# Performance work log

Measured on AMD Instinct MI355X. Metric: run time of the kernel, lower is better.

Reference implementation:

```python
import jax, jax.numpy as jnp
import numpy as np

B, T, E, H = 1024, 200, 128, 128
N_ITEMS, N_CATS = 100000, 1000
LN_EPS = 1e-5


def _prelu(x, a):
    return jnp.where(x >= 0, x, a * x)


def _layernorm(x, g, b):
    m = x.mean(-1, keepdims=True)
    v = ((x - m) ** 2).mean(-1, keepdims=True)
    return (x - m) / jnp.sqrt(v + LN_EPS) * g + b


def setup_inputs() -> dict:
    key = jax.random.key(0)
    it = iter(jax.random.split(key, 64))
    nx = lambda: next(it)
    def lin(out_d, in_d):
        s = 1.0 / np.sqrt(in_d)
        return jax.random.uniform(nx(), (out_d, in_d), jnp.float32, -s, s)
    inp = {}
    inp['behavior_ids'] = jax.random.randint(nx(), (B, T), 0, N_ITEMS)
    inp['candidate_id'] = jax.random.randint(nx(), (B,), 0, N_ITEMS)
    inp['candidate_cat'] = jax.random.randint(nx(), (B,), 0, N_CATS)
    inp['dense_features'] = jax.random.normal(nx(), (B, 5), jnp.float32)
    inp['item_emb'] = (jax.random.normal(nx(), (N_ITEMS, E), jnp.float32) * 0.01).at[0].set(0.0)
    inp['cat_emb'] = (jax.random.normal(nx(), (N_CATS, E // 2), jnp.float32) * 0.01).at[0].set(0.0)
    # nn.GRU params (gate order r,z,n)
    inp['gru_wih'] = lin(3 * H, E)
    inp['gru_whh'] = lin(3 * H, H)
    inp['gru_bih'] = jnp.zeros((3 * H,), jnp.float32)
    inp['gru_bhh'] = jnp.zeros((3 * H,), jnp.float32)
    # auxiliary_net: Linear(H,E) -> ReLU -> Linear(E,1)
    inp['aux_w1'] = lin(E, H); inp['aux_b1'] = jnp.zeros((E,), jnp.float32)
    inp['aux_w2'] = lin(1, E); inp['aux_b2'] = jnp.zeros((1,), jnp.float32)
    # attention_mlp: Linear(3H,64) -> PReLU -> Linear(64,1)
    inp['att_w1'] = lin(64, 3 * H); inp['att_b1'] = jnp.zeros((64,), jnp.float32)
    inp['att_a'] = jnp.array(0.25, jnp.float32)
    inp['att_w2'] = lin(1, 64); inp['att_b2'] = jnp.zeros((1,), jnp.float32)
    # AUGRU gates: Linear(2H, H) each
    inp['wz'] = lin(H, 2 * H); inp['bz'] = jnp.zeros((H,), jnp.float32)
    inp['wr'] = lin(H, 2 * H); inp['br'] = jnp.zeros((H,), jnp.float32)
    inp['wh'] = lin(H, 2 * H); inp['bh'] = jnp.zeros((H,), jnp.float32)
    # dense_proj Linear(5,32)
    inp['dp_w'] = lin(32, 5); inp['dp_b'] = jnp.zeros((32,), jnp.float32)
    # MLP: 352 -> 256 -> 128 -> 64, each Linear + LayerNorm + PReLU
    dims = [H + E + E // 2 + 32, 256, 128, 64]
    for i in range(3):
        inp[f'm_w{i+1}'] = lin(dims[i + 1], dims[i])
        inp[f'm_b{i+1}'] = jnp.zeros((dims[i + 1],), jnp.float32)
        inp[f'ln_g{i+1}'] = jnp.ones((dims[i + 1],), jnp.float32)
        inp[f'ln_b{i+1}'] = jnp.zeros((dims[i + 1],), jnp.float32)
        inp[f'pa{i+1}'] = jnp.array(0.25, jnp.float32)
    # 3 task heads Linear(64,1), stacked
    inp['heads_w'] = lin(3, 64); inp['heads_b'] = jnp.zeros((3,), jnp.float32)
    return inp


def _forward_core(behavior_ids, candidate_id, candidate_cat, dense_features,
                  item_emb, cat_emb, gru_wih, gru_whh, gru_bih, gru_bhh,
                  aux_w1, aux_b1, aux_w2, aux_b2,
                  att_w1, att_b1, att_a, att_w2, att_b2,
                  wz, bz, wr, br, wh, bh, dp_w, dp_b,
                  m_w1, m_b1, ln_g1, ln_b1, pa1,
                  m_w2, m_b2, ln_g2, ln_b2, pa2,
                  m_w3, m_b3, ln_g3, ln_b3, pa3,
                  heads_w, heads_b):
    beh = item_emb[behavior_ids]            # [B,T,E]
    cand = item_emb[candidate_id]           # [B,E]
    catv = cat_emb[candidate_cat]           # [B,E//2]
    Bsz = beh.shape[0]
    Hd = gru_whh.shape[1]
    h0 = jnp.zeros((Bsz, Hd), beh.dtype)
    # --- interest extractor GRU (cuDNN GRU math, gate order r,z,n) ---
    xp = jnp.einsum('bte,ge->btg', beh, gru_wih) + gru_bih  # [B,T,3H]
    def gru_step(h, x):
        hp = h @ gru_whh.T + gru_bhh
        xr, xz, xn = jnp.split(x, 3, -1)
        hr, hz, hn = jnp.split(hp, 3, -1)
        r = jax.nn.sigmoid(xr + hr)
        z = jax.nn.sigmoid(xz + hz)
        n = jnp.tanh(xn + r * hn)
        hnew = (1 - z) * n + z * h
        return hnew, hnew
    _, hs = jax.lax.scan(gru_step, h0, jnp.swapaxes(xp, 0, 1))
    hs = jnp.swapaxes(hs, 0, 1)             # [B,T,H]
    # --- auxiliary logits ---
    aux = jax.nn.relu(hs[:, :-1] @ aux_w1.T + aux_b1) @ aux_w2.T + aux_b2  # [B,T-1,1]
    # --- attention (embed_dim == hidden_size so cand_proj == candidate_emb) ---
    ce = cand[:, None, :]
    att_in = jnp.concatenate([hs, jnp.broadcast_to(ce, hs.shape), hs * ce], -1)  # [B,T,3H]
    scores = (_prelu(att_in @ att_w1.T + att_b1, att_a) @ att_w2.T + att_b2)[..., 0]
    att = jax.nn.softmax(scores, axis=-1)   # [B,T]
    # --- AUGRU: attention-modulated update gate ---
    def augru_step(h, xs):
        x, a = xs                           # x: [B,H], a: [B]
        comb = jnp.concatenate([x, h], -1)
        z = jax.nn.sigmoid(comb @ wz.T + bz)
        r = jax.nn.sigmoid(comb @ wr.T + br)
        comb_r = jnp.concatenate([x, r * h], -1)
        ht = jnp.tanh(comb_r @ wh.T + bh)
        zp = a[:, None] * z
        return (1 - zp) * h + zp * ht, None
    hT, _ = jax.lax.scan(augru_step, h0, (jnp.swapaxes(hs, 0, 1), att.T))
    # --- fusion MLP (dropout is identity in eval) ---
    dense_out = dense_features @ dp_w.T + dp_b
    x = jnp.concatenate([hT, cand, catv, dense_out], -1)  # [B,352]
    for (w, b, g, be, a) in ((m_w1, m_b1, ln_g1, ln_b1, pa1),
                             (m_w2, m_b2, ln_g2, ln_b2, pa2),
                             (m_w3, m_b3, ln_g3, ln_b3, pa3)):
        x = _prelu(_layernorm(x @ w.T + b, g, be), a)
    preds = jax.nn.sigmoid(x @ heads_w.T + heads_b)  # [B,3] == 3 heads of [B,1]
    return preds, aux


def reference(behavior_ids, candidate_id, candidate_cat, dense_features,
              item_emb, cat_emb, gru_wih, gru_whh, gru_bih, gru_bhh,
              aux_w1, aux_b1, aux_w2, aux_b2,
              att_w1, att_b1, att_a, att_w2, att_b2,
              wz, bz, wr, br, wh, bh, dp_w, dp_b,
              m_w1, m_b1, ln_g1, ln_b1, pa1,
              m_w2, m_b2, ln_g2, ln_b2, pa2,
              m_w3, m_b3, ln_g3, ln_b3, pa3,
              heads_w, heads_b):
    return _forward_core(behavior_ids, candidate_id, candidate_cat, dense_features,
                         item_emb, cat_emb, gru_wih, gru_whh, gru_bih, gru_bhh,
                         aux_w1, aux_b1, aux_w2, aux_b2,
                         att_w1, att_b1, att_a, att_w2, att_b2,
                         wz, bz, wr, br, wh, bh, dp_w, dp_b,
                         m_w1, m_b1, ln_g1, ln_b1, pa1,
                         m_w2, m_b2, ln_g2, ln_b2, pa2,
                         m_w3, m_b3, ln_g3, ln_b3, pa3,
                         heads_w, heads_b)
```

## Files before the change

### kernel.cpp

```cpp
#include <hip/hip_runtime.h>


typedef __bf16 bf16;
typedef float f32x4 __attribute__((ext_vector_type(4)));
typedef __bf16 bf16x8 __attribute__((ext_vector_type(8)));
typedef __bf16 bf16x4 __attribute__((ext_vector_type(4)));

#define MFMA16(a, b, c) __builtin_amdgcn_mfma_f32_16x16x32_bf16((a), (b), (c), 0, 0, 0)

#define BATCH 1024
#define SEQT 200
#define F32_ONE 0x3F800000u

__device__ __forceinline__ float sigm(float x) {
  return __builtin_amdgcn_rcpf(1.0f + __expf(-x));
}
__device__ __forceinline__ float tanh_fast(float x) {
  float ax = fabsf(x);
  float t = 1.0f - 2.0f * __builtin_amdgcn_rcpf(__expf(2.0f * ax) + 1.0f);
  return copysignf(t, x);
}

__device__ __forceinline__ void bar_lgkm() {
  asm volatile("s_waitcnt lgkmcnt(0)\n\ts_barrier" ::: "memory");
}

__device__ __forceinline__ void dma16(const void* g, void* l) {
  __builtin_amdgcn_global_load_lds((__attribute__((address_space(1))) void*)g,
                                   (__attribute__((address_space(3))) void*)l,
                                   16, 0, 0);
}

template <typename DT> __device__ __forceinline__ float ldf(const DT* p, long i);
template <> __device__ __forceinline__ float ldf<bf16>(const bf16* p, long i) { return (float)p[i]; }
template <> __device__ __forceinline__ float ldf<float>(const float* p, long i) { return p[i]; }

template <typename DT> __device__ __forceinline__ bf16x8 ld8(const DT* p, long i);
template <> __device__ __forceinline__ bf16x8 ld8<bf16>(const bf16* p, long i) {
  return *(const bf16x8*)(p + i);
}
template <> __device__ __forceinline__ bf16x8 ld8<float>(const float* p, long i) {
  f32x4 a = *(const f32x4*)(p + i);
  f32x4 b = *(const f32x4*)(p + i + 4);
  bf16x8 r;
  r[0] = (bf16)a[0]; r[1] = (bf16)a[1]; r[2] = (bf16)a[2]; r[3] = (bf16)a[3];
  r[4] = (bf16)b[0]; r[5] = (bf16)b[1]; r[6] = (bf16)b[2]; r[7] = (bf16)b[3];
  return r;
}

template <typename DT>
__device__ __forceinline__ void prep_body(
    const int* __restrict__ cid, const int* __restrict__ ccat,
    const DT* __restrict__ dense, const DT* __restrict__ item_emb,
    const DT* __restrict__ cat_emb, const DT* __restrict__ dp_w,
    const DT* __restrict__ dp_b, bf16* __restrict__ candbuf, bf16* __restrict__ xf) {
  const int b = blockIdx.x;
  const int t = threadIdx.x;
  bf16 v = (bf16)ldf(item_emb, (long)cid[b] * 128 + t);
  candbuf[b * 128 + t] = v;
  xf[(long)b * 352 + 128 + t] = v;
  if (t < 64) xf[(long)b * 352 + 256 + t] = (bf16)ldf(cat_emb, (long)ccat[b] * 64 + t);
  if (t < 32) {
    float s = ldf(dp_b, t);
    for (int k = 0; k < 5; k++) s += ldf(dense, b * 5 + k) * ldf(dp_w, t * 5 + k);
    xf[(long)b * 352 + 320 + t] = (bf16)s;
  }
}
__global__ __launch_bounds__(128) void k_prep(
    const unsigned* __restrict__ disc, const int* cid, const int* ccat,
    const void* dense, const void* item_emb, const void* cat_emb,
    const void* dp_w, const void* dp_b, bf16* candbuf, bf16* xf) {
  if (*disc == F32_ONE)
    prep_body<float>(cid, ccat, (const float*)dense, (const float*)item_emb,
                     (const float*)cat_emb, (const float*)dp_w, (const float*)dp_b, candbuf, xf);
  else
    prep_body<bf16>(cid, ccat, (const bf16*)dense, (const bf16*)item_emb,
                    (const bf16*)cat_emb, (const bf16*)dp_w, (const bf16*)dp_b, candbuf, xf);
}

template <typename DT>
__device__ __forceinline__ void gru3_body(
    const int* __restrict__ ids, const DT* __restrict__ item_emb,
    const DT* __restrict__ wih, const DT* __restrict__ whh,
    const DT* __restrict__ bih, const DT* __restrict__ bhh, bf16* __restrict__ hs,
    bf16 (*hA)[16][136], bf16 (*xb)[4][16][136], char* raw) {
  const int b0 = blockIdx.x * 16;
  const int tid = threadIdx.x;
  const int w = tid >> 6, lane = tid & 63, l15 = lane & 15, quad = lane >> 4;
  const int nc = w * 16 + l15;

  for (int i = tid; i < 2 * 16 * 136; i += 512) ((bf16*)hA)[i] = (bf16)0.0f;

  bf16x8 wir[4], wiz[4], win_[4], whr[4], whz[4], whn[4];
#pragma unroll
  for (int k = 0; k < 4; k++) {
    const long off = k * 32 + quad * 8;
    wir[k] = ld8(wih, (long)nc * 128 + off);
    wiz[k] = ld8(wih, (long)(128 + nc) * 128 + off);
    win_[k] = ld8(wih, (long)(256 + nc) * 128 + off);
    whr[k] = ld8(whh, (long)nc * 128 + off);
    whz[k] = ld8(whh, (long)(128 + nc) * 128 + off);
    whn[k] = ld8(whh, (long)(256 + nc) * 128 + off);
  }
  const float br_s = ldf(bih, nc) + ldf(bhh, nc);
  const float bz_s = ldf(bih, 128 + nc) + ldf(bhh, 128 + nc);
  const float bxn_s = ldf(bih, 256 + nc);
  const float bhn_s = ldf(bhh, 256 + nc);

  const int idrow = (sizeof(DT) == 4) ? (tid >> 5) : ((tid >> 4) & 15);
  const int* idbase = ids + (long)(b0 + idrow) * SEQT;

  auto DMA = [&](const int4 id4) {
    if constexpr (sizeof(DT) == 4) {
#pragma unroll
      for (int j = 0; j < 4; j++)
        dma16((const char*)(item_emb + (long)((&id4.x)[j]) * 128) + (tid & 31) * 16,
              raw + (j * 512 + tid) * 16);
    } else {
#pragma unroll
      for (int j = 0; j < 2; j++) {
        const int slot = j * 2 + (tid >> 8);
        dma16((const char*)(item_emb + (long)((&id4.x)[slot]) * 128) + (tid & 15) * 16,
              raw + (j * 512 + tid) * 16);
      }
    }
  };
  auto CONV = [&](int buf) {
    if constexpr (sizeof(DT) == 4) {
      const float* rf = (const float*)raw;
#pragma unroll
      for (int h = 0; h < 4; h++) {
        const int e = h * 2048 + tid * 4;
        f32x4 a = *(const f32x4*)(rf + e);
        const int slot = e >> 11, row = (e >> 7) & 15, col = e & 127;
        bf16x4 o;
        o[0] = (bf16)a[0]; o[1] = (bf16)a[1]; o[2] = (bf16)a[2]; o[3] = (bf16)a[3];
        *(bf16x4*)&xb[buf][slot][row][col] = o;
      }
    } else {
      const bf16* rh = (const bf16*)raw;
#pragma unroll
      for (int h = 0; h < 2; h++) {
        const int e = h * 4096 + tid * 8;
        const int slot = e >> 11, row = (e >> 7) & 15, col = e & 127;
        *(bf16x8*)&xb[buf][slot][row][col] = *(const bf16x8*)(rh + e);
      }
    }
  };

  const int srow = tid >> 5, sch = (tid & 31) * 4;
  bf16* hsb = hs + ((long)(b0 + srow) * SEQT) * 128 + sch;

  float hreg[4] = {0.f, 0.f, 0.f, 0.f};
  const f32x4 z4 = {0.f, 0.f, 0.f, 0.f};

  int4 idv = *(const int4*)(idbase);
  DMA(idv);
  idv = *(const int4*)(idbase + 4);
  asm volatile("s_waitcnt vmcnt(1)" ::: "memory");
  __builtin_amdgcn_sched_barrier(0);
  __builtin_amdgcn_s_barrier();
  CONV(0);
  asm volatile("s_waitcnt lgkmcnt(0)" ::: "memory");
  __builtin_amdgcn_sched_barrier(0);
  __builtin_amdgcn_s_barrier();
  DMA(idv);
  idv = *(const int4*)(idbase + 8);

#define GRU_STEP(P, S)                                                         \
  {                                                                            \
    const int tt = t0 + (S);                                                   \
    bf16x8 af[4], xaf[4];                                                      \
    _Pragma("unroll") for (int k = 0; k < 4; k++) {                            \
      af[k] = *(const bf16x8*)&hA[P][l15][k * 32 + quad * 8];                  \
      xaf[k] = *(const bf16x8*)&xb[buf][S][l15][k * 32 + quad * 8];            \
    }                                                                          \
    { const int slot = tt ? tt - 1 : 0;                                        \
      bf16x4 hv = *(const bf16x4*)&hA[P][srow][sch];                           \
      *(bf16x4*)(hsb + (long)slot * 128) = hv; }                               \
    f32x4 ar = z4, az = z4, axn = z4, ahn = z4;                                \
    _Pragma("unroll") for (int k = 0; k < 4; k++) {                            \
      ar = MFMA16(xaf[k], wir[k], ar);                                         \
      az = MFMA16(xaf[k], wiz[k], az);                                         \
      axn = MFMA16(xaf[k], win_[k], axn);                                      \
    }                                                                          \
    _Pragma("unroll") for (int k = 0; k < 4; k++) {                            \
      ar = MFMA16(af[k], whr[k], ar);                                          \
      az = MFMA16(af[k], whz[k], az);                                          \
      ahn = MFMA16(af[k], whn[k], ahn);                                        \
    }                                                                          \
    _Pragma("unroll") for (int r = 0; r < 4; r++) {                            \
      float r_ = sigm(ar[r] + br_s);                                           \
      float z_ = sigm(az[r] + bz_s);                                           \
      float n_ = tanh_fast(axn[r] + bxn_s + r_ * (ahn[r] + bhn_s));            \
      float hnew = (1.0f - z_) * n_ + z_ * hreg[r];                            \
      hreg[r] = hnew;                                                          \
      hA[(P) ^ 1][quad * 4 + r][nc] = (bf16)hnew;                              \
    }                                                                          \
    bar_lgkm();                                                                \
  }

  for (int c = 0; c < 50; c++) {
    const int t0 = c * 4;
    const int buf = c & 1;
    GRU_STEP(0, 0) GRU_STEP(1, 1) GRU_STEP(0, 2) GRU_STEP(1, 3)
    if (c < 49) {
      asm volatile("s_waitcnt vmcnt(4)" ::: "memory");
      __builtin_amdgcn_sched_barrier(0);
      __builtin_amdgcn_s_barrier();
      CONV((c + 1) & 1);
      asm volatile("s_waitcnt lgkmcnt(0)" ::: "memory");
      __builtin_amdgcn_sched_barrier(0);
      __builtin_amdgcn_s_barrier();
      if (c < 48) {
        DMA(idv);
        int nid = (c + 3) * 4; if (nid > 196) nid = 196;
        idv = *(const int4*)(idbase + nid);
      }
    }
  }
#undef GRU_STEP
  { bf16x4 hv = *(const bf16x4*)&hA[0][srow][sch];
    *(bf16x4*)(hsb + (long)(SEQT - 1) * 128) = hv; }
}
__global__ __launch_bounds__(512, 1) void k_gru3(
    const unsigned* __restrict__ disc, const int* ids, const void* item_emb,
    const void* wih, const void* whh, const void* bih, const void* bhh, bf16* hs) {
  __shared__ __align__(16) bf16 hA[2][16][136];
  __shared__ __align__(16) bf16 xb[2][4][16][136];
  __shared__ __align__(16) char raw[32768];
  if (*disc == F32_ONE)
    gru3_body<float>(ids, (const float*)item_emb, (const float*)wih, (const float*)whh,
                     (const float*)bih, (const float*)bhh, hs, hA, xb, raw);
  else
    gru3_body<bf16>(ids, (const bf16*)item_emb, (const bf16*)wih, (const bf16*)whh,
                    (const bf16*)bih, (const bf16*)bhh, hs, hA, xb, raw);
}

template <typename DT>
__device__ __forceinline__ void augru3_body(
    const bf16* __restrict__ hsrc, const float* __restrict__ att,
    const DT* __restrict__ wz, const DT* __restrict__ wr, const DT* __restrict__ wh,
    const DT* __restrict__ bzv, const DT* __restrict__ brv, const DT* __restrict__ bhv,
    bf16* __restrict__ xf_out,
    bf16 (*hA)[16][136], bf16 (*rhA)[136], float (*attL)[201],
    bf16 (*xb)[4][16][136], char* raw) {
  const int b0 = blockIdx.x * 16;
  const int tid = threadIdx.x;
  const int w = tid >> 6, lane = tid & 63, l15 = lane & 15, quad = lane >> 4;
  const int nc = w * 16 + l15;

  for (int i = tid; i < 2 * 16 * 136; i += 512) ((bf16*)hA)[i] = (bf16)0.0f;
  for (int i = tid; i < 16 * SEQT; i += 512) {
    int r = i / SEQT, c = i - r * SEQT;
    attL[r][c] = att[(long)(b0 + r) * SEQT + c];
  }

  bf16x8 wzx[4], wzh[4], wrx[4], wrh[4], whx[4], whh_[4];
#pragma unroll
  for (int k = 0; k < 4; k++) {
    const long off = k * 32 + quad * 8;
    wzx[k] = ld8(wz, (long)nc * 256 + off);
    wzh[k] = ld8(wz, (long)nc * 256 + 128 + off);
    wrx[k] = ld8(wr, (long)nc * 256 + off);
    wrh[k] = ld8(wr, (long)nc * 256 + 128 + off);
    whx[k] = ld8(wh, (long)nc * 256 + off);
    whh_[k] = ld8(wh, (long)nc * 256 + 128 + off);
  }
  const float bz_s = ldf(bzv, nc);
  const float br_s = ldf(brv, nc);
  const float bh_s = ldf(bhv, nc);

  auto DMA = [&](int t0) {
#pragma unroll
    for (int j = 0; j < 2; j++) {
      const int slot = j * 2 + (tid >> 8);
      const int row = (tid >> 4) & 15;
      const bf16* src = hsrc + ((long)(b0 + row) * SEQT + t0 + slot) * 128 + (tid & 15) * 8;
      dma16(src, raw + (j * 512 + tid) * 16);
    }
  };
  auto CONV = [&](int buf) {
    const bf16* rh = (const bf16*)raw;
#pragma unroll
    for (int h = 0; h < 2; h++) {
      const int e = h * 4096 + tid * 8;
      const int slot = e >> 11, row = (e >> 7) & 15, col = e & 127;
      *(bf16x8*)&xb[buf][slot][row][col] = *(const bf16x8*)(rh + e);
    }
  };

  float hreg[4] = {0.f, 0.f, 0.f, 0.f};
  const f32x4 z4 = {0.f, 0.f, 0.f, 0.f};

  DMA(0);
  asm volatile("s_waitcnt vmcnt(0)" ::: "memory");
  __builtin_amdgcn_sched_barrier(0);
  __builtin_amdgcn_s_barrier();
  CONV(0);
  asm volatile("s_waitcnt lgkmcnt(0)" ::: "memory");
  __builtin_amdgcn_sched_barrier(0);
  __builtin_amdgcn_s_barrier();
  DMA(4);

#define AUGRU_STEP(P, S)                                                       \
  {                                                                            \
    const int tt = t0 + (S);                                                   \
    bf16x8 af[4], xaf[4];                                                      \
    _Pragma("unroll") for (int k = 0; k < 4; k++) {                            \
      af[k] = *(const bf16x8*)&hA[P][l15][k * 32 + quad * 8];                  \
      xaf[k] = *(const bf16x8*)&xb[buf][S][l15][k * 32 + quad * 8];            \
    }                                                                          \
    f32x4 az = z4, ar = z4, axh = z4;                                          \
    _Pragma("unroll") for (int k = 0; k < 4; k++) {                            \
      az = MFMA16(xaf[k], wzx[k], az);                                         \
      ar = MFMA16(xaf[k], wrx[k], ar);                                         \
      axh = MFMA16(xaf[k], whx[k], axh);                                       \
    }                                                                          \
    _Pragma("unroll") for (int k = 0; k < 4; k++) {                            \
      az = MFMA16(af[k], wzh[k], az);                                          \
      ar = MFMA16(af[k], wrh[k], ar);                                          \
    }                                                                          \
    float zp[4];                                                               \
    _Pragma("unroll") for (int r = 0; r < 4; r++) {                            \
      float a_ = attL[quad * 4 + r][tt];                                       \
      float z_ = sigm(az[r] + bz_s);                                           \
      float r_ = sigm(ar[r] + br_s);                                           \
      zp[r] = a_ * z_;                                                         \
      rhA[quad * 4 + r][nc] = (bf16)(r_ * hreg[r]);                            \
    }                                                                          \
    bar_lgkm();                                                                \
    bf16x8 rf[4];                                                              \
    _Pragma("unroll") for (int k = 0; k < 4; k++)                              \
      rf[k] = *(const bf16x8*)&rhA[l15][k * 32 + quad * 8];                    \
    f32x4 ahh = axh;                                                           \
    _Pragma("unroll") for (int k = 0; k < 4; k++)                              \
      ahh = MFMA16(rf[k], whh_[k], ahh);                                       \
    _Pragma("unroll") for (int r = 0; r < 4; r++) {                            \
      float ht = tanh_fast(ahh[r] + bh_s);                                     \
      float hnew = (1.f - zp[r]) * hreg[r] + zp[r] * ht;                       \
      hreg[r] = hnew;                                                          \
      hA[(P) ^ 1][quad * 4 + r][nc] = (bf16)hnew;                              \
    }                                                                          \
    bar_lgkm();                                                                \
  }

  for (int c = 0; c < 50; c++) {
    const int t0 = c * 4;
    const int buf = c & 1;
    AUGRU_STEP(0, 0) AUGRU_STEP(1, 1) AUGRU_STEP(0, 2) AUGRU_STEP(1, 3)
    if (c < 49) {
      asm volatile("s_waitcnt vmcnt(0)" ::: "memory");
      __builtin_amdgcn_sched_barrier(0);
      __builtin_amdgcn_s_barrier();
      CONV((c + 1) & 1);
      asm volatile("s_waitcnt lgkmcnt(0)" ::: "memory");
      __builtin_amdgcn_sched_barrier(0);
      __builtin_amdgcn_s_barrier();
      if (c < 48) DMA((c + 2) * 4);
    }
  }
#undef AUGRU_STEP
#pragma unroll
  for (int r = 0; r < 4; r++)
    xf_out[(long)(b0 + quad * 4 + r) * 352 + nc] = (bf16)hreg[r];
}
__global__ __launch_bounds__(512, 1) void k_augru3(
    const unsigned* __restrict__ disc, const bf16* hsrc, const float* att,
    const void* wz, const void* wr, const void* wh,
    const void* bzv, const void* brv, const void* bhv, bf16* xf_out) {
  __shared__ __align__(16) bf16 hA[2][16][136];
  __shared__ __align__(16) bf16 rhA[16][136];
  __shared__ __align__(16) float attL[16][201];
  __shared__ __align__(16) bf16 xb[2][4][16][136];
  __shared__ __align__(16) char raw[16384];
  if (*disc == F32_ONE)
    augru3_body<float>(hsrc, att, (const float*)wz, (const float*)wr, (const float*)wh,
                       (const float*)bzv, (const float*)brv, (const float*)bhv, xf_out,
                       hA, rhA, attL, xb, raw);
  else
    augru3_body<bf16>(hsrc, att, (const bf16*)wz, (const bf16*)wr, (const bf16*)wh,
                      (const bf16*)bzv, (const bf16*)brv, (const bf16*)bhv, xf_out,
                      hA, rhA, attL, xb, raw);
}

template <typename DT>
__device__ __forceinline__ void aux_body(
    const bf16* __restrict__ hs, const DT* __restrict__ w1, const DT* __restrict__ b1v,
    const DT* __restrict__ w2v, const DT* __restrict__ b2v, float* __restrict__ outaux,
    bf16 (*As)[136], bf16 (*Ws)[136]) {
  const int bg = blockIdx.y;
  const int t0 = blockIdx.x * 64;
  const int tid = threadIdx.x;
  const int w = tid >> 6, lane = tid & 63, l15 = lane & 15, quad = lane >> 4;
#pragma unroll
  for (int j = 0; j < 8; j++) {
    int ci = j * 256 + tid;
    int row = ci >> 4, k8 = (ci & 15) * 8;
    *(bf16x8*)&Ws[row][k8] = ld8(w1, (long)row * 128 + k8);
  }
  float b1c[8], w2c[8];
#pragma unroll
  for (int nt = 0; nt < 8; nt++) {
    int n = nt * 16 + l15;
    b1c[nt] = ldf(b1v, n);
    w2c[nt] = ldf(w2v, n);
  }
  const float b2 = ldf(b2v, 0);
  const f32x4 z4 = {0.f, 0.f, 0.f, 0.f};
  __syncthreads();

  for (int bi = 0; bi < 16; bi++) {
    const int b = bg * 16 + bi;
#pragma unroll
    for (int j = 0; j < 4; j++) {
      int ci = j * 256 + tid;
      int row = ci >> 4, k8 = (ci & 15) * 8;
      int t = t0 + row; int tc = t < 199 ? t : 198;
      *(bf16x8*)&As[row][k8] = *(const bf16x8*)(hs + ((long)b * SEQT + tc) * 128 + k8);
    }
    bar_lgkm();
    bf16x8 af[4];
#pragma unroll
    for (int k = 0; k < 4; k++) af[k] = *(const bf16x8*)&As[w * 16 + l15][k * 32 + quad * 8];
    float part[4] = {0.f, 0.f, 0.f, 0.f};
#pragma unroll
    for (int nt = 0; nt < 8; nt++) {
      f32x4 acc = z4;
#pragma unroll
      for (int k = 0; k < 4; k++) {
        bf16x8 bfr = *(const bf16x8*)&Ws[nt * 16 + l15][k * 32 + quad * 8];
        acc = MFMA16(af[k], bfr, acc);
      }
#pragma unroll
      for (int r = 0; r < 4; r++) {
        float y = acc[r] + b1c[nt];
        part[r] += (y > 0.f ? y : 0.f) * w2c[nt];
      }
    }
#pragma unroll
    for (int m = 1; m < 16; m <<= 1)
#pragma unroll
      for (int r = 0; r < 4; r++) part[r] += __shfl_xor(part[r], m, 64);
    if (l15 == 0) {
#pragma unroll
      for (int r = 0; r < 4; r++) {
        int t = t0 + w * 16 + quad * 4 + r;
        if (t < 199) outaux[(long)b * 199 + t] = part[r] + b2;
      }
    }
    bar_lgkm();
  }
}
__global__ __launch_bounds__(256) void k_aux(
    const unsigned* __restrict__ disc, const bf16* hs, const void* w1, const void* b1v,
    const void* w2v, const void* b2v, float* outaux) {
  __shared__ bf16 As[64][136];
  __shared__ bf16 Ws[128][136];
  if (*disc == F32_ONE)
    aux_body<float>(hs, (const float*)w1, (const float*)b1v, (const float*)w2v,
                    (const float*)b2v, outaux, As, Ws);
  else
    aux_body<bf16>(hs, (const bf16*)w1, (const bf16*)b1v, (const bf16*)w2v,
                   (const bf16*)b2v, outaux, As, Ws);
}

template <typename DT>
__device__ __forceinline__ void att_body(
    const bf16* __restrict__ hs, const bf16* __restrict__ cand,
    const DT* __restrict__ w1, const DT* __restrict__ b1v, const DT* __restrict__ a_s,
    const DT* __restrict__ w2v, const DT* __restrict__ b2v, float* __restrict__ scores,
    bf16 (*As)[392], bf16 (*Ws)[392]) {
  const int bg = blockIdx.y;
  const int t0 = blockIdx.x * 64;
  const int tid = threadIdx.x;
  const int w = tid >> 6, lane = tid & 63, l15 = lane & 15, quad = lane >> 4;
#pragma unroll
  for (int j = 0; j < 12; j++) {
    int ci = j * 256 + tid;
    int row = ci / 48;
    int k8 = (ci % 48) * 8;
    *(bf16x8*)&Ws[row][k8] = ld8(w1, (long)row * 384 + k8);
  }
  const float aP = ldf(a_s, 0);
  const float b2 = ldf(b2v, 0);
  float b1c[4], w2c[4];
#pragma unroll
  for (int nt = 0; nt < 4; nt++) {
    int n = nt * 16 + l15;
    b1c[nt] = ldf(b1v, n);
    w2c[nt] = ldf(w2v, n);
  }
  const f32x4 z4 = {0.f, 0.f, 0.f, 0.f};
  __syncthreads();

  for (int bi = 0; bi < 16; bi++) {
    const int b = bg * 16 + bi;
#pragma unroll
    for (int j = 0; j < 12; j++) {
      int ci = j * 256 + tid;
      int row = ci / 48;
      int k8 = (ci % 48) * 8;
      int t = t0 + row; int tc = t < SEQT ? t : SEQT - 1;
      const bf16* hrow = hs + ((long)b * SEQT + tc) * 128;
      bf16x8 v;
      if (k8 < 128) v = *(const bf16x8*)(hrow + k8);
      else if (k8 < 256) v = *(const bf16x8*)(cand + b * 128 + (k8 - 128));
      else {
        bf16x8 hv = *(const bf16x8*)(hrow + (k8 - 256));
        bf16x8 cv = *(const bf16x8*)(cand + b * 128 + (k8 - 256));
#pragma unroll
        for (int q = 0; q < 8; q++) v[q] = (bf16)((float)hv[q] * (float)cv[q]);
      }
      *(bf16x8*)&As[row][k8] = v;
    }
    bar_lgkm();
    f32x4 acc[4] = {z4, z4, z4, z4};
    for (int k = 0; k < 12; k++) {
      bf16x8 af = *(const bf16x8*)&As[w * 16 + l15][k * 32 + quad * 8];
#pragma unroll
      for (int nt = 0; nt < 4; nt++) {
        bf16x8 bfr = *(const bf16x8*)&Ws[nt * 16 + l15][k * 32 + quad * 8];
        acc[nt] = MFMA16(af, bfr, acc[nt]);
      }
    }
    float part[4] = {0.f, 0.f, 0.f, 0.f};
#pragma unroll
    for (int nt = 0; nt < 4; nt++) {
#pragma unroll
      for (int r = 0; r < 4; r++) {
        float y = acc[nt][r] + b1c[nt];
        y = (y >= 0.f) ? y : aP * y;
        part[r] += y * w2c[nt];
      }
    }
#pragma unroll
    for (int m = 1; m < 16; m <<= 1)
#pragma unroll
      for (int r = 0; r < 4; r++) part[r] += __shfl_xor(part[r], m, 64);
    if (l15 == 0) {
#pragma unroll
      for (int r = 0; r < 4; r++) {
        int t = t0 + w * 16 + quad * 4 + r;
        if (t < SEQT) scores[(long)b * SEQT + t] = part[r] + b2;
      }
    }
    bar_lgkm();
  }
}
__global__ __launch_bounds__(256) void k_att(
    const unsigned* __restrict__ disc, const bf16* hs, const bf16* cand,
    const void* w1, const void* b1v, const void* a_s,
    const void* w2v, const void* b2v, float* scores) {
  __shared__ bf16 As[64][392];
  __shared__ bf16 Ws[64][392];
  if (*disc == F32_ONE)
    att_body<float>(hs, cand, (const float*)w1, (const float*)b1v, (const float*)a_s,
                    (const float*)w2v, (const float*)b2v, scores, As, Ws);
  else
    att_body<bf16>(hs, cand, (const bf16*)w1, (const bf16*)b1v, (const bf16*)a_s,
                   (const bf16*)w2v, (const bf16*)b2v, scores, As, Ws);
}

__global__ __launch_bounds__(256) void k_softmax(float* __restrict__ sc) {
  const int b = blockIdx.x, tid = threadIdx.x;
  __shared__ float red[256];
  float v = (tid < SEQT) ? sc[(long)b * SEQT + tid] : -1e30f;
  red[tid] = v; __syncthreads();
  for (int s = 128; s > 0; s >>= 1) { if (tid < s) red[tid] = fmaxf(red[tid], red[tid + s]); __syncthreads(); }
  float mx = red[0]; __syncthreads();
  float e = (tid < SEQT) ? __expf(v - mx) : 0.f;
  red[tid] = e; __syncthreads();
  for (int s = 128; s > 0; s >>= 1) { if (tid < s) red[tid] += red[tid + s]; __syncthreads(); }
  float inv = 1.0f / red[0];
  if (tid < SEQT) sc[(long)b * SEQT + tid] = e * inv;
}

template <typename DT>
__device__ __forceinline__ void mlp_body(
    const bf16* __restrict__ xf,
    const DT* __restrict__ w1, const DT* __restrict__ b1, const DT* __restrict__ g1, const DT* __restrict__ be1, const DT* __restrict__ pa1,
    const DT* __restrict__ w2, const DT* __restrict__ b2, const DT* __restrict__ g2, const DT* __restrict__ be2, const DT* __restrict__ pa2,
    const DT* __restrict__ w3, const DT* __restrict__ b3, const DT* __restrict__ g3, const DT* __restrict__ be3, const DT* __restrict__ pa3,
    const DT* __restrict__ hw, const DT* __restrict__ hb, float* __restrict__ preds,
    float (*xs)[352], float (*ys)[256]) {
  const int tid = threadIdx.x, w = tid >> 6, lane = tid & 63;
  const int b = blockIdx.x * 4 + w;
  for (int i = lane; i < 352; i += 64) xs[w][i] = (float)xf[(long)b * 352 + i];
  __syncthreads();
  float acc1[4];
#pragma unroll
  for (int oi = 0; oi < 4; oi++) {
    int o = lane + 64 * oi;
    float s = ldf(b1, o);
    for (int k = 0; k < 352; k += 8) {
      bf16x8 wv = ld8(w1, (long)o * 352 + k);
#pragma unroll
      for (int j = 0; j < 8; j++) s += xs[w][k + j] * (float)wv[j];
    }
    acc1[oi] = s;
  }
  float sm = acc1[0] + acc1[1] + acc1[2] + acc1[3];
#pragma unroll
  for (int m = 1; m < 64; m <<= 1) sm += __shfl_xor(sm, m, 64);
  float mean = sm * (1.0f / 256.0f);
  float vs = 0.f;
#pragma unroll
  for (int oi = 0; oi < 4; oi++) { float d = acc1[oi] - mean; vs += d * d; }
#pragma unroll
  for (int m = 1; m < 64; m <<= 1) vs += __shfl_xor(vs, m, 64);
  float rstd = rsqrtf(vs * (1.0f / 256.0f) + 1e-5f);
  float a1 = ldf(pa1, 0);
#pragma unroll
  for (int oi = 0; oi < 4; oi++) {
    int o = lane + 64 * oi;
    float y = (acc1[oi] - mean) * rstd * ldf(g1, o) + ldf(be1, o);
    ys[w][o] = (y >= 0.f) ? y : a1 * y;
  }
  __syncthreads();
  float acc2[2];
#pragma unroll
  for (int oi = 0; oi < 2; oi++) {
    int o = lane + 64 * oi;
    float s = ldf(b2, o);
    for (int k = 0; k < 256; k += 8) {
      bf16x8 wv = ld8(w2, (long)o * 256 + k);
#pragma unroll
      for (int j = 0; j < 8; j++) s += ys[w][k + j] * (float)wv[j];
    }
    acc2[oi] = s;
  }
  sm = acc2[0] + acc2[1];
#pragma unroll
  for (int m = 1; m < 64; m <<= 1) sm += __shfl_xor(sm, m, 64);
  mean = sm * (1.0f / 128.0f);
  vs = 0.f;
#pragma unroll
  for (int oi = 0; oi < 2; oi++) { float d = acc2[oi] - mean; vs += d * d; }
#pragma unroll
  for (int m = 1; m < 64; m <<= 1) vs += __shfl_xor(vs, m, 64);
  rstd = rsqrtf(vs * (1.0f / 128.0f) + 1e-5f);
  float a2 = ldf(pa2, 0);
  __syncthreads();
#pragma unroll
  for (int oi = 0; oi < 2; oi++) {
    int o = lane + 64 * oi;
    float y = (acc2[oi] - mean) * rstd * ldf(g2, o) + ldf(be2, o);
    xs[w][o] = (y >= 0.f) ? y : a2 * y;
  }
  __syncthreads();
  float s3 = ldf(b3, lane);
  for (int k = 0; k < 128; k += 8) {
    bf16x8 wv = ld8(w3, (long)lane * 128 + k);
#pragma unroll
    for (int j = 0; j < 8; j++) s3 += xs[w][k + j] * (float)wv[j];
  }
  sm = s3;
#pragma unroll
  for (int m = 1; m < 64; m <<= 1) sm += __shfl_xor(sm, m, 64);
  mean = sm * (1.0f / 64.0f);
  float d3 = s3 - mean;
  vs = d3 * d3;
#pragma unroll
  for (int m = 1; m < 64; m <<= 1) vs += __shfl_xor(vs, m, 64);
  rstd = rsqrtf(vs * (1.0f / 64.0f) + 1e-5f);
  float a3 = ldf(pa3, 0);
  float y3 = d3 * rstd * ldf(g3, lane) + ldf(be3, lane);
  y3 = (y3 >= 0.f) ? y3 : a3 * y3;
  ys[w][lane] = y3;
  __syncthreads();
  if (lane < 3) {
    float s = ldf(hb, lane);
    for (int k = 0; k < 64; k++) s += ys[w][k] * ldf(hw, lane * 64 + k);
    preds[(long)b * 3 + lane] = sigm(s);
  }
}
__global__ __launch_bounds__(256) void k_mlp(
    const unsigned* __restrict__ disc, const bf16* xf,
    const void* w1, const void* b1, const void* g1, const void* be1, const void* pa1,
    const void* w2, const void* b2, const void* g2, const void* be2, const void* pa2,
    const void* w3, const void* b3, const void* g3, const void* be3, const void* pa3,
    const void* hw, const void* hb, float* preds) {
  __shared__ float xs[4][352];
  __shared__ float ys[4][256];
  if (*disc == F32_ONE)
    mlp_body<float>(xf,
        (const float*)w1, (const float*)b1, (const float*)g1, (const float*)be1, (const float*)pa1,
        (const float*)w2, (const float*)b2, (const float*)g2, (const float*)be2, (const float*)pa2,
        (const float*)w3, (const float*)b3, (const float*)g3, (const float*)be3, (const float*)pa3,
        (const float*)hw, (const float*)hb, preds, xs, ys);
  else
    mlp_body<bf16>(xf,
        (const bf16*)w1, (const bf16*)b1, (const bf16*)g1, (const bf16*)be1, (const bf16*)pa1,
        (const bf16*)w2, (const bf16*)b2, (const bf16*)g2, (const bf16*)be2, (const bf16*)pa2,
        (const bf16*)w3, (const bf16*)b3, (const bf16*)g3, (const bf16*)be3, (const bf16*)pa3,
        (const bf16*)hw, (const bf16*)hb, preds, xs, ys);
}

extern "C" void kernel_launch(void* const* d_in, const int* in_sizes, int n_in,
                              void* d_out, int out_size, void* d_ws, size_t ws_size,
                              hipStream_t stream) {
  const int* behavior_ids = (const int*)d_in[0];
  const int* candidate_id = (const int*)d_in[1];
  const int* candidate_cat = (const int*)d_in[2];
  const void* dense = d_in[3];
  const void* item_emb = d_in[4];
  const void* cat_emb = d_in[5];
  const void* gru_wih = d_in[6];
  const void* gru_whh = d_in[7];
  const void* gru_bih = d_in[8];
  const void* gru_bhh = d_in[9];
  const void* aux_w1 = d_in[10];
  const void* aux_b1 = d_in[11];
  const void* aux_w2 = d_in[12];
  const void* aux_b2 = d_in[13];
  const void* att_w1 = d_in[14];
  const void* att_b1 = d_in[15];
  const void* att_a = d_in[16];
  const void* att_w2 = d_in[17];
  const void* att_b2 = d_in[18];
  const void* wz = d_in[19];
  const void* bz = d_in[20];
  const void* wr = d_in[21];
  const void* br = d_in[22];
  const void* wh = d_in[23];
  const void* bh = d_in[24];
  const void* dp_w = d_in[25];
  const void* dp_b = d_in[26];
  const void* m_w1 = d_in[27];
  const void* m_b1 = d_in[28];
  const void* ln_g1 = d_in[29];
  const void* ln_b1 = d_in[30];
  const void* pa1 = d_in[31];
  const void* m_w2 = d_in[32];
  const void* m_b2 = d_in[33];
  const void* ln_g2 = d_in[34];
  const void* ln_b2 = d_in[35];
  const void* pa2 = d_in[36];
  const void* m_w3 = d_in[37];
  const void* m_b3 = d_in[38];
  const void* ln_g3 = d_in[39];
  const void* ln_b3 = d_in[40];
  const void* pa3 = d_in[41];
  const void* heads_w = d_in[42];
  const void* heads_b = d_in[43];
  (void)in_sizes; (void)n_in; (void)out_size; (void)ws_size;

  const unsigned* disc = (const unsigned*)ln_g1;

  char* ws = (char*)d_ws;
  bf16* HS = (bf16*)(ws);
  float* SC = (float*)(ws + 52428800L);
  bf16* CAND = (bf16*)(ws + 53248000L);
  bf16* XF = (bf16*)(ws + 53510144L);
  float* OUT = (float*)d_out;

  k_prep<<<BATCH, 128, 0, stream>>>(disc, candidate_id, candidate_cat, dense, item_emb,
                                    cat_emb, dp_w, dp_b, CAND, XF);
  k_gru3<<<64, 512, 0, stream>>>(disc, behavior_ids, item_emb, gru_wih, gru_whh,
                                 gru_bih, gru_bhh, HS);
  k_aux<<<dim3(4, 64), 256, 0, stream>>>(disc, HS, aux_w1, aux_b1, aux_w2, aux_b2, OUT + 3072);
  k_att<<<dim3(4, 64), 256, 0, stream>>>(disc, HS, CAND, att_w1, att_b1, att_a, att_w2, att_b2, SC);
  k_softmax<<<BATCH, 256, 0, stream>>>(SC);
  k_augru3<<<64, 512, 0, stream>>>(disc, HS, SC, wz, wr, wh, bz, br, bh, XF);
  k_mlp<<<256, 256, 0, stream>>>(disc, XF,
      m_w1, m_b1, ln_g1, ln_b1, pa1,
      m_w2, m_b2, ln_g2, ln_b2, pa2,
      m_w3, m_b3, ln_g3, ln_b3, pa3,
      heads_w, heads_b, OUT);
}
```

Before: 831.4 us.

## Fuse attention-score and auxiliary-net kernels with register-resident weights and double-buffered DMA

Merges the separate aux-net and attention-MLP kernels into one kernel that loads each hidden-state tile once and computes both heads from it. Weights stay in registers instead of LDS, and the hidden-state tiles are double-buffered through async DMA into an XOR-swizzled LDS layout. The candidate embedding is read straight from item_emb by id rather than from the precomputed CAND buffer. The point is to cut duplicate HS reads, LDS traffic and one launch, at the cost of higher register pressure.

```diff
diff --git a/kernel.cpp b/kernel.cpp
--- a/kernel.cpp
+++ b/kernel.cpp
@@ -238,6 +238,163 @@
 }
 
 template <typename DT>
+__device__ __forceinline__ void attaux_body(
+    const bf16* __restrict__ hs, const int* __restrict__ cid,
+    const DT* __restrict__ item_emb,
+    const DT* __restrict__ aw1, const DT* __restrict__ ab1,
+    const DT* __restrict__ aw2, const DT* __restrict__ ab2,
+    const DT* __restrict__ tw1, const DT* __restrict__ tb1, const DT* __restrict__ ta,
+    const DT* __restrict__ tw2, const DT* __restrict__ tb2,
+    float* __restrict__ sc, float* __restrict__ outaux,
+    bf16 (*As)[64][128], float (*scPt)[64], float (*scPa)[64]) {
+  const int t0 = blockIdx.x * 64;
+  const int b0 = blockIdx.y * 16;
+  const int tid = threadIdx.x, w = tid >> 6, lane = tid & 63, l15 = lane & 15, quad = lane >> 4;
+
+  const int tn = w * 16 + l15;
+  bf16x8 wth[4], wtc[4], wthc[4], wa0[4], wa1[4];
+#pragma unroll
+  for (int k = 0; k < 4; k++) {
+    const long off = k * 32 + quad * 8;
+    wth[k]  = ld8(tw1, (long)tn * 384 + off);
+    wtc[k]  = ld8(tw1, (long)tn * 384 + 128 + off);
+    wthc[k] = ld8(tw1, (long)tn * 384 + 256 + off);
+    wa0[k]  = ld8(aw1, (long)((2 * w) * 16 + l15) * 128 + off);
+    wa1[k]  = ld8(aw1, (long)((2 * w + 1) * 16 + l15) * 128 + off);
+  }
+  const float tb1c = ldf(tb1, tn), tw2c = ldf(tw2, tn);
+  const float ab1c0 = ldf(ab1, (2 * w) * 16 + l15), aw2c0 = ldf(aw2, (2 * w) * 16 + l15);
+  const float ab1c1 = ldf(ab1, (2 * w + 1) * 16 + l15), aw2c1 = ldf(aw2, (2 * w + 1) * 16 + l15);
+  const float aP = ldf(ta, 0), tb2s = ldf(tb2, 0), ab2s = ldf(ab2, 0);
+
+  auto DMA = [&](int b, int buf) {
+#pragma unroll
+    for (int c = 0; c < 4; c++) {
+      const int idx = c * 256 + tid;
+      const int row = idx >> 4, p = idx & 15;
+      int t = t0 + row; if (t > SEQT - 1) t = SEQT - 1;
+      const bf16* src = hs + ((long)b * SEQT + t) * 128 + ((p ^ (row & 7)) * 8);
+      dma16(src, (char*)(&As[buf][0][0]) + idx * 16);
+    }
+  };
+  auto CANDLD = [&](int b, bf16x8* cf) {
+#pragma unroll
+    for (int k = 0; k < 4; k++)
+      cf[k] = ld8(item_emb, (long)cid[b] * 128 + k * 32 + quad * 8);
+  };
+
+  const f32x4 z4 = {0.f, 0.f, 0.f, 0.f};
+  bf16x8 candA[4], candB[4];
+  DMA(b0, 0);
+  CANDLD(b0, candA);
+  asm volatile("s_waitcnt vmcnt(0)" ::: "memory");
+  __builtin_amdgcn_sched_barrier(0);
+  __builtin_amdgcn_s_barrier();
+
+#define AA_STEP(BI, CUSE, CPF)                                                 \
+  {                                                                            \
+    const int b = b0 + (BI);                                                   \
+    const int buf = (BI) & 1;                                                  \
+    if ((BI) + 1 < 16) { DMA(b + 1, buf ^ 1); CANDLD(b + 1, CPF); }            \
+    _Pragma("unroll") for (int m = 0; m < 4; m++) {                            \
+      const bf16* arow = &As[buf][m * 16 + l15][0];                            \
+      bf16x8 af[4], hcf[4];                                                    \
+      _Pragma("unroll") for (int k = 0; k < 4; k++)                            \
+        af[k] = *(const bf16x8*)((const char*)arow +                           \
+                                 (((k * 4 + quad) ^ (l15 & 7)) << 4));         \
+      _Pragma("unroll") for (int k = 0; k < 4; k++)                            \
+      _Pragma("unroll") for (int j = 0; j < 8; j++)                            \
+        hcf[k][j] = (bf16)((float)af[k][j] * (float)CUSE[k][j]);               \
+      f32x4 at = z4, aa0 = z4, aa1 = z4;                                       \
+      _Pragma("unroll") for (int k = 0; k < 4; k++) {                          \
+        at = MFMA16(af[k], wth[k], at);                                        \
+        at = MFMA16(CUSE[k], wtc[k], at);                                      \
+        at = MFMA16(hcf[k], wthc[k], at);                                      \
+        aa0 = MFMA16(af[k], wa0[k], aa0);                                      \
+        aa1 = MFMA16(af[k], wa1[k], aa1);                                      \
+      }                                                                        \
+      float tp[4], ap[4];                                                      \
+      _Pragma("unroll") for (int r = 0; r < 4; r++) {                          \
+        float y = at[r] + tb1c;                                                \
+        y = (y >= 0.f) ? y : aP * y;                                           \
+        tp[r] = y * tw2c;                                                      \
+        float y0 = aa0[r] + ab1c0;                                             \
+        float y1 = aa1[r] + ab1c1;                                             \
+        ap[r] = (y0 > 0.f ? y0 : 0.f) * aw2c0 + (y1 > 0.f ? y1 : 0.f) * aw2c1; \
+      }                                                                        \
+      _Pragma("unroll") for (int mm = 1; mm < 16; mm <<= 1)                    \
+      _Pragma("unroll") for (int r = 0; r < 4; r++) {                          \
+        tp[r] += __shfl_xor(tp[r], mm, 64);                                    \
+        ap[r] += __shfl_xor(ap[r], mm, 64);                                    \
+      }                                                                        \
+      if (l15 == 0) {                                                          \
+        *(float4*)&scPt[w][m * 16 + quad * 4] =                                \
+            make_float4(tp[0], tp[1], tp[2], tp[3]);                           \
+        *(float4*)&scPa[w][m * 16 + quad * 4] =                                \
+            make_float4(ap[0], ap[1], ap[2], ap[3]);                           \
+      }                                                                        \
+    }                                                                          \
+    bar_lgkm();                                                                \
+    if (tid < 64) {                                                            \
+      int t = t0 + tid;                                                        \
+      if (t < SEQT) {                                                          \
+        float s = scPt[0][tid] + scPt[1][tid] + scPt[2][tid] + scPt[3][tid];   \
+        sc[(long)b * SEQT + t] = s + tb2s;                                     \
+      }                                                                        \
+    } else if (tid < 128) {                                                    \
+      int tt2 = tid - 64, t = t0 + tt2;                                        \
+      if (t < SEQT - 1) {                                                      \
+        float s = scPa[0][tt2] + scPa[1][tt2] + scPa[2][tt2] + scPa[3][tt2];   \
+        outaux[(long)b * 199 + t] = s + ab2s;                                  \
+      }                                                                        \
+    }                                                                          \
+    asm volatile("s_waitcnt vmcnt(0) lgkmcnt(0)" ::: "memory");                \
+    __builtin_amdgcn_sched_barrier(0);                                         \
+    __builtin_amdgcn_s_barrier();                                              \
+  }
+
+  for (int bi = 0; bi < 16; bi += 2) {
+    AA_STEP(bi, candA, candB)
+    AA_STEP(bi + 1, candB, candA)
+  }
+#undef AA_STEP
+}
+__global__ __launch_bounds__(256, 1) void k_attaux(
+    const unsigned* __restrict__ disc, const bf16* hs, const int* cid,
+    const void* item_emb,
+    const void* aw1, const void* ab1, const void* aw2, const void* ab2,
+    const void* tw1, const void* tb1, const void* ta, const void* tw2, const void* tb2,
+    float* sc, float* outaux) {
+  __shared__ __align__(16) bf16 As[2][64][128];
+  __shared__ __align__(16) float scPt[4][64];
+  __shared__ __align__(16) float scPa[4][64];
+  if (*disc == F32_ONE)
+    attaux_body<float>(hs, cid, (const float*)item_emb,
+                       (const float*)aw1, (const float*)ab1, (const float*)aw2, (const float*)ab2,
+                       (const float*)tw1, (const float*)tb1, (const float*)ta,
+                       (const float*)tw2, (const float*)tb2, sc, outaux, As, scPt, scPa);
+  else
+    attaux_body<bf16>(hs, cid, (const bf16*)item_emb,
+                      (const bf16*)aw1, (const bf16*)ab1, (const bf16*)aw2, (const bf16*)ab2,
+                      (const bf16*)tw1, (const bf16*)tb1, (const bf16*)ta,
+                      (const bf16*)tw2, (const bf16*)tb2, sc, outaux, As, scPt, scPa);
+}
+
+__global__ __launch_bounds__(256) void k_softmax(float* __restrict__ sc) {
+  const int b = blockIdx.x, tid = threadIdx.x;
+  __shared__ float red[256];
+  float v = (tid < SEQT) ? sc[(long)b * SEQT + tid] : -1e30f;
+  red[tid] = v; __syncthreads();
+  for (int s = 128; s > 0; s >>= 1) { if (tid < s) red[tid] = fmaxf(red[tid], red[tid + s]); __syncthreads(); }
+  float mx = red[0]; __syncthreads();
+  float e = (tid < SEQT) ? __expf(v - mx) : 0.f;
+  red[tid] = e; __syncthreads();
+  for (int s = 128; s > 0; s >>= 1) { if (tid < s) red[tid] += red[tid + s]; __syncthreads(); }
+  float inv = 1.0f / red[0];
+  if (tid < SEQT) sc[(long)b * SEQT + tid] = e * inv;
+}
+
+template <typename DT>
 __device__ __forceinline__ void augru3_body(
     const bf16* __restrict__ hsrc, const float* __restrict__ att,
     const DT* __restrict__ wz, const DT* __restrict__ wr, const DT* __restrict__ wh,
@@ -382,198 +539,6 @@
     augru3_body<bf16>(hsrc, att, (const bf16*)wz, (const bf16*)wr, (const bf16*)wh,
                       (const bf16*)bzv, (const bf16*)brv, (const bf16*)bhv, xf_out,
                       hA, rhA, attL, xb, raw);
-}
-
-template <typename DT>
-__device__ __forceinline__ void aux_body(
-    const bf16* __restrict__ hs, const DT* __restrict__ w1, const DT* __restrict__ b1v,
-    const DT* __restrict__ w2v, const DT* __restrict__ b2v, float* __restrict__ outaux,
-    bf16 (*As)[136], bf16 (*Ws)[136]) {
-  const int bg = blockIdx.y;
-  const int t0 = blockIdx.x * 64;
-  const int tid = threadIdx.x;
-  const int w = tid >> 6, lane = tid & 63, l15 = lane & 15, quad = lane >> 4;
-#pragma unroll
-  for (int j = 0; j < 8; j++) {
-    int ci = j * 256 + tid;
-    int row = ci >> 4, k8 = (ci & 15) * 8;
-    *(bf16x8*)&Ws[row][k8] = ld8(w1, (long)row * 128 + k8);
-  }
-  float b1c[8], w2c[8];
-#pragma unroll
-  for (int nt = 0; nt < 8; nt++) {
-    int n = nt * 16 + l15;
-    b1c[nt] = ldf(b1v, n);
-    w2c[nt] = ldf(w2v, n);
-  }
-  const float b2 = ldf(b2v, 0);
-  const f32x4 z4 = {0.f, 0.f, 0.f, 0.f};
-  __syncthreads();
-
-  for (int bi = 0; bi < 16; bi++) {
-    const int b = bg * 16 + bi;
-#pragma unroll
-    for (int j = 0; j < 4; j++) {
-      int ci = j * 256 + tid;
-      int row = ci >> 4, k8 = (ci & 15) * 8;
-      int t = t0 + row; int tc = t < 199 ? t : 198;
-      *(bf16x8*)&As[row][k8] = *(const bf16x8*)(hs + ((long)b * SEQT + tc) * 128 + k8);
-    }
-    bar_lgkm();
-    bf16x8 af[4];
-#pragma unroll
-    for (int k = 0; k < 4; k++) af[k] = *(const bf16x8*)&As[w * 16 + l15][k * 32 + quad * 8];
-    float part[4] = {0.f, 0.f, 0.f, 0.f};
-#pragma unroll
-    for (int nt = 0; nt < 8; nt++) {
-      f32x4 acc = z4;
-#pragma unroll
-      for (int k = 0; k < 4; k++) {
-        bf16x8 bfr = *(const bf16x8*)&Ws[nt * 16 + l15][k * 32 + quad * 8];
-        acc = MFMA16(af[k], bfr, acc);
-      }
-#pragma unroll
-      for (int r = 0; r < 4; r++) {
-        float y = acc[r] + b1c[nt];
-        part[r] += (y > 0.f ? y : 0.f) * w2c[nt];
-      }
-    }
-#pragma unroll
-    for (int m = 1; m < 16; m <<= 1)
-#pragma unroll
-      for (int r = 0; r < 4; r++) part[r] += __shfl_xor(part[r], m, 64);
-    if (l15 == 0) {
-#pragma unroll
-      for (int r = 0; r < 4; r++) {
-        int t = t0 + w * 16 + quad * 4 + r;
-        if (t < 199) outaux[(long)b * 199 + t] = part[r] + b2;
-      }
-    }
-    bar_lgkm();
-  }
-}
-__global__ __launch_bounds__(256) void k_aux(
-    const unsigned* __restrict__ disc, const bf16* hs, const void* w1, const void* b1v,
-    const void* w2v, const void* b2v, float* outaux) {
-  __shared__ bf16 As[64][136];
-  __shared__ bf16 Ws[128][136];
-  if (*disc == F32_ONE)
-    aux_body<float>(hs, (const float*)w1, (const float*)b1v, (const float*)w2v,
-                    (const float*)b2v, outaux, As, Ws);
-  else
-    aux_body<bf16>(hs, (const bf16*)w1, (const bf16*)b1v, (const bf16*)w2v,
-                   (const bf16*)b2v, outaux, As, Ws);
-}
-
-template <typename DT>
-__device__ __forceinline__ void att_body(
-    const bf16* __restrict__ hs, const bf16* __restrict__ cand,
-    const DT* __restrict__ w1, const DT* __restrict__ b1v, const DT* __restrict__ a_s,
-    const DT* __restrict__ w2v, const DT* __restrict__ b2v, float* __restrict__ scores,
-    bf16 (*As)[392], bf16 (*Ws)[392]) {
-  const int bg = blockIdx.y;
-  const int t0 = blockIdx.x * 64;
-  const int tid = threadIdx.x;
-  const int w = tid >> 6, lane = tid & 63, l15 = lane & 15, quad = lane >> 4;
-#pragma unroll
-  for (int j = 0; j < 12; j++) {
-    int ci = j * 256 + tid;
-    int row = ci / 48;
-    int k8 = (ci % 48) * 8;
-    *(bf16x8*)&Ws[row][k8] = ld8(w1, (long)row * 384 + k8);
-  }
-  const float aP = ldf(a_s, 0);
-  const float b2 = ldf(b2v, 0);
-  float b1c[4], w2c[4];
-#pragma unroll
-  for (int nt = 0; nt < 4; nt++) {
-    int n = nt * 16 + l15;
-    b1c[nt] = ldf(b1v, n);
-    w2c[nt] = ldf(w2v, n);
-  }
-  const f32x4 z4 = {0.f, 0.f, 0.f, 0.f};
-  __syncthreads();
-
-  for (int bi = 0; bi < 16; bi++) {
-    const int b = bg * 16 + bi;
-#pragma unroll
-    for (int j = 0; j < 12; j++) {
-      int ci = j * 256 + tid;
-      int row = ci / 48;
-      int k8 = (ci % 48) * 8;
-      int t = t0 + row; int tc = t < SEQT ? t : SEQT - 1;
-      const bf16* hrow = hs + ((long)b * SEQT + tc) * 128;
-      bf16x8 v;
-      if (k8 < 128) v = *(const bf16x8*)(hrow + k8);
-      else if (k8 < 256) v = *(const bf16x8*)(cand + b * 128 + (k8 - 128));
-      else {
-        bf16x8 hv = *(const bf16x8*)(hrow + (k8 - 256));
-        bf16x8 cv = *(const bf16x8*)(cand + b * 128 + (k8 - 256));
-#pragma unroll
-        for (int q = 0; q < 8; q++) v[q] = (bf16)((float)hv[q] * (float)cv[q]);
-      }
-      *(bf16x8*)&As[row][k8] = v;
-    }
-    bar_lgkm();
-    f32x4 acc[4] = {z4, z4, z4, z4};
-    for (int k = 0; k < 12; k++) {
-      bf16x8 af = *(const bf16x8*)&As[w * 16 + l15][k * 32 + quad * 8];
-#pragma unroll
-      for (int nt = 0; nt < 4; nt++) {
-        bf16x8 bfr = *(const bf16x8*)&Ws[nt * 16 + l15][k * 32 + quad * 8];
-        acc[nt] = MFMA16(af, bfr, acc[nt]);
-      }
-    }
-    float part[4] = {0.f, 0.f, 0.f, 0.f};
-#pragma unroll
-    for (int nt = 0; nt < 4; nt++) {
-#pragma unroll
-      for (int r = 0; r < 4; r++) {
-        float y = acc[nt][r] + b1c[nt];
-        y = (y >= 0.f) ? y : aP * y;
-        part[r] += y * w2c[nt];
-      }
-    }
-#pragma unroll
-    for (int m = 1; m < 16; m <<= 1)
-#pragma unroll
-      for (int r = 0; r < 4; r++) part[r] += __shfl_xor(part[r], m, 64);
-    if (l15 == 0) {
-#pragma unroll
-      for (int r = 0; r < 4; r++) {
-        int t = t0 + w * 16 + quad * 4 + r;
-        if (t < SEQT) scores[(long)b * SEQT + t] = part[r] + b2;
-      }
-    }
-    bar_lgkm();
-  }
-}
-__global__ __launch_bounds__(256) void k_att(
-    const unsigned* __restrict__ disc, const bf16* hs, const bf16* cand,
-    const void* w1, const void* b1v, const void* a_s,
-    const void* w2v, const void* b2v, float* scores) {
-  __shared__ bf16 As[64][392];
-  __shared__ bf16 Ws[64][392];
-  if (*disc == F32_ONE)
-    att_body<float>(hs, cand, (const float*)w1, (const float*)b1v, (const float*)a_s,
-                    (const float*)w2v, (const float*)b2v, scores, As, Ws);
-  else
-    att_body<bf16>(hs, cand, (const bf16*)w1, (const bf16*)b1v, (const bf16*)a_s,
-                   (const bf16*)w2v, (const bf16*)b2v, scores, As, Ws);
-}
-
-__global__ __launch_bounds__(256) void k_softmax(float* __restrict__ sc) {
-  const int b = blockIdx.x, tid = threadIdx.x;
-  __shared__ float red[256];
-  float v = (tid < SEQT) ? sc[(long)b * SEQT + tid] : -1e30f;
-  red[tid] = v; __syncthreads();
-  for (int s = 128; s > 0; s >>= 1) { if (tid < s) red[tid] = fmaxf(red[tid], red[tid + s]); __syncthreads(); }
-  float mx = red[0]; __syncthreads();
-  float e = (tid < SEQT) ? __expf(v - mx) : 0.f;
-  red[tid] = e; __syncthreads();
-  for (int s = 128; s > 0; s >>= 1) { if (tid < s) red[tid] += red[tid + s]; __syncthreads(); }
-  float inv = 1.0f / red[0];
-  if (tid < SEQT) sc[(long)b * SEQT + tid] = e * inv;
 }
 
 template <typename DT>
@@ -759,8 +724,10 @@
                                     cat_emb, dp_w, dp_b, CAND, XF);
   k_gru3<<<64, 512, 0, stream>>>(disc, behavior_ids, item_emb, gru_wih, gru_whh,
                                  gru_bih, gru_bhh, HS);
-  k_aux<<<dim3(4, 64), 256, 0, stream>>>(disc, HS, aux_w1, aux_b1, aux_w2, aux_b2, OUT + 3072);
-  k_att<<<dim3(4, 64), 256, 0, stream>>>(disc, HS, CAND, att_w1, att_b1, att_a, att_w2, att_b2, SC);
+  k_attaux<<<dim3(4, 64), 256, 0, stream>>>(disc, HS, candidate_id, item_emb,
+                                            aux_w1, aux_b1, aux_w2, aux_b2,
+                                            att_w1, att_b1, att_a, att_w2, att_b2,
+                                            SC, OUT + 3072);
   k_softmax<<<BATCH, 256, 0, stream>>>(SC);
   k_augru3<<<64, 512, 0, stream>>>(disc, HS, SC, wz, wr, wh, bz, br, bh, XF);
   k_mlp<<<256, 256, 0, stream>>>(disc, XF,
```

Measured after the change: 727.2 us. 12.5% less time.
